# Optimization experiments

Measured on AMD Instinct MI355X. Metric: run time of the kernel, lower is better.

The kernel has to match this reference:

```python
import jax, jax.numpy as jnp
import numpy as np

N_NODE, N_USER, N_PRICE, EMB = 100000, 40000, 100, 128
E_VV, E_VP, E_VU, E_UV = 2000000, 200000, 2000000, 2000000


def _spmm(rows, cols, vals, x, n_rows):
    # sparse COO (n_rows, n_cols) @ x  -> (n_rows, d)
    return jax.ops.segment_sum(vals[:, None] * x[cols], rows, num_segments=n_rows)


def _row_norm_spmm(rows, cols, vals, x, n_rows):
    # torch.sparse.mm followed by division by row-sum of values (+1e-8)
    num = _spmm(rows, cols, vals, x, n_rows)
    den = jax.ops.segment_sum(vals, rows, num_segments=n_rows)[:, None] + 1e-8
    return num / den


def _linear(x, W, b):
    return x @ W.T + b


def setup_inputs() -> dict:
    key = jax.random.key(0)
    ks = jax.random.split(key, 40)
    d = {}
    d['embedding'] = jax.random.normal(ks[0], (N_NODE, EMB), jnp.float32) * 0.1
    d['pri_emb'] = jax.random.normal(ks[1], (N_PRICE, EMB), jnp.float32) * 0.1
    d['user_emb'] = jax.random.normal(ks[2], (N_USER, EMB), jnp.float32) * 0.1
    d['adj_rows'] = jax.random.randint(ks[3], (E_VV,), 0, N_NODE, jnp.int32)
    d['adj_cols'] = jax.random.randint(ks[4], (E_VV,), 0, N_NODE, jnp.int32)
    d['adj_vals'] = jax.random.uniform(ks[5], (E_VV,), jnp.float32)
    d['vp_rows'] = jax.random.randint(ks[6], (E_VP,), 0, N_NODE, jnp.int32)
    d['vp_cols'] = jax.random.randint(ks[7], (E_VP,), 0, N_PRICE, jnp.int32)
    d['vp_vals'] = jax.random.uniform(ks[8], (E_VP,), jnp.float32)
    d['vu_rows'] = jax.random.randint(ks[9], (E_VU,), 0, N_NODE, jnp.int32)
    d['vu_cols'] = jax.random.randint(ks[10], (E_VU,), 0, N_USER, jnp.int32)
    d['vu_vals'] = jax.random.uniform(ks[11], (E_VU,), jnp.float32)
    d['pv_rows'] = jax.random.randint(ks[12], (E_VP,), 0, N_PRICE, jnp.int32)
    d['pv_cols'] = jax.random.randint(ks[13], (E_VP,), 0, N_NODE, jnp.int32)
    d['pv_vals'] = jax.random.uniform(ks[14], (E_VP,), jnp.float32)
    d['uv_rows'] = jax.random.randint(ks[15], (E_UV,), 0, N_USER, jnp.int32)
    d['uv_cols'] = jax.random.randint(ks[16], (E_UV,), 0, N_NODE, jnp.int32)
    d['uv_vals'] = jax.random.uniform(ks[17], (E_UV,), jnp.float32)
    d['item_price_indices'] = jax.random.randint(ks[18], (N_NODE,), 0, N_PRICE, jnp.int32)
    s = 0.02
    d['mat_vu'] = jax.random.normal(ks[19], (N_NODE, 1), jnp.float32) * s
    d['mat_pv'] = jax.random.normal(ks[20], (N_PRICE, 1), jnp.float32) * s
    d['mat_uv'] = jax.random.normal(ks[21], (N_USER, 1), jnp.float32) * s
    d['W_aogi'] = jax.random.normal(ks[22], (EMB, 2 * EMB), jnp.float32) * s
    d['b_aogi'] = jnp.zeros((EMB,), jnp.float32)
    d['W_bgi1'] = jax.random.normal(ks[23], (EMB, EMB), jnp.float32) * s
    d['b_bgi1'] = jnp.zeros((EMB,), jnp.float32)
    d['W_aogp'] = jax.random.normal(ks[24], (EMB, 2 * EMB), jnp.float32) * s
    d['b_aogp'] = jnp.zeros((EMB,), jnp.float32)
    d['W_bgp1'] = jax.random.normal(ks[25], (EMB, EMB), jnp.float32) * s
    d['b_bgp1'] = jnp.zeros((EMB,), jnp.float32)
    d['W_user'] = jax.random.normal(ks[26], (EMB, 3 * EMB), jnp.float32) * s
    d['b_user'] = jnp.zeros((EMB,), jnp.float32)
    d['user_lambda'] = jnp.asarray(0.2, jnp.float32)
    return d


def _forward(embedding, pri_emb, user_emb,
             adj_rows, adj_cols, adj_vals,
             vp_rows, vp_cols, vp_vals,
             vu_rows, vu_cols, vu_vals,
             pv_rows, pv_cols, pv_vals,
             uv_rows, uv_cols, uv_vals,
             item_price_indices,
             mat_vu, mat_pv, mat_uv,
             W_aogi, b_aogi, W_bgi1, b_bgi1,
             W_aogp, b_aogp, W_bgp1, b_bgp1,
             W_user, b_user, user_lambda,
             layers=1):
    def inter_gate(Wa, ba, Wb, bb, e1, e2):
        gate = jax.nn.sigmoid(_linear(jnp.concatenate([e1, e2], 1), Wa, ba) + _linear(e1, Wb, bb))
        return e1 + gate * e2  # dropout50 = identity at eval

    def intra_gate(rows, cols, vals, mat_v, emb2, n_rows):
        # torch version computes the chunked row-normalized spmm under no_grad
        alpha = jax.lax.stop_gradient(_row_norm_spmm(rows, cols, vals, emb2, n_rows))
        return alpha * mat_v  # dropout70 = identity at eval

    for _ in range(layers):
        item = (inter_gate(W_aogi, b_aogi, W_bgi1, b_bgi1, embedding,
                           _spmm(vp_rows, vp_cols, vp_vals, pri_emb, N_NODE))
                + _spmm(adj_rows, adj_cols, adj_vals, embedding, N_NODE)
                + user_lambda * intra_gate(vu_rows, vu_cols, vu_vals, mat_vu, user_emb, N_NODE))
        price = inter_gate(W_aogp, b_aogp, W_bgp1, b_bgp1, pri_emb,
                           intra_gate(pv_rows, pv_cols, pv_vals, mat_pv, embedding, N_PRICE))
        e_price_user = _spmm(uv_rows, uv_cols, uv_vals, pri_emb[item_price_indices], N_USER)
        e_item_user = intra_gate(uv_rows, uv_cols, uv_vals, mat_uv, embedding, N_USER)
        gate = jax.nn.sigmoid(_linear(jnp.concatenate([user_emb, e_item_user, e_price_user], -1), W_user, b_user))
        user = gate * user_emb + (1.0 - gate) * e_item_user
        embedding, pri_emb, user_emb = item, price, user
    return item, price, user


def reference(embedding, pri_emb, user_emb,
              adj_rows, adj_cols, adj_vals,
              vp_rows, vp_cols, vp_vals,
              vu_rows, vu_cols, vu_vals,
              pv_rows, pv_cols, pv_vals,
              uv_rows, uv_cols, uv_vals,
              item_price_indices,
              mat_vu, mat_pv, mat_uv,
              W_aogi, b_aogi, W_bgi1, b_bgi1,
              W_aogp, b_aogp, W_bgp1, b_bgp1,
              W_user, b_user, user_lambda):
    return _forward(embedding, pri_emb, user_emb,
                    adj_rows, adj_cols, adj_vals,
                    vp_rows, vp_cols, vp_vals,
                    vu_rows, vu_cols, vu_vals,
                    pv_rows, pv_cols, pv_vals,
                    uv_rows, uv_cols, uv_vals,
                    item_price_indices,
                    mat_vu, mat_pv, mat_uv,
                    W_aogi, b_aogi, W_bgi1, b_bgi1,
                    W_aogp, b_aogp, W_bgp1, b_bgp1,
                    W_user, b_user, user_lambda)
```

## Files before the change

### kernel.cpp

```cpp
#include <hip/hip_runtime.h>
#include <hip/hip_bf16.h>

#define N_NODE 100000
#define N_USER 40000
#define N_PRICE 100
#define EMB 128
#define E_VV 2000000
#define E_VP 200000
#define E_VU 2000000
#define E_UV 2000000

#define FOFF0 0
#define FOFF1 256
#define FOFF2 512
#define FOFF3 767
#define FOFF4 1023
#define FTOT  1073
#define EPB   8192
#define BK1 245
#define BK2 490
#define BK3 735
#define BK4 760
#define BKT 785
#define CB1 256
#define CB2 512
#define CB3 767
#define CB4 1023
#define CBT 1073
#define RB_PV   100
#define RB_ITEM 25000
#define RB_USER 10000
#define RBT (RB_PV + RB_ITEM + RB_USER)
#define FB_ITEM 782
#define FB_USER 313
#define FBT (FB_ITEM + FB_USER + 50)

typedef __attribute__((ext_vector_type(8))) short short8;
typedef __attribute__((ext_vector_type(4))) float f32x4;

__device__ __forceinline__ float sigf(float x){ return 1.f/(1.f+__expf(-x)); }
__device__ __forceinline__ unsigned bfr(float f){
  unsigned u = __float_as_uint(f);
  return (u + 0x7FFFu + ((u>>16)&1u)) >> 16;
}
__device__ __forceinline__ float bf_lo(unsigned u){ return __uint_as_float(u << 16); }
__device__ __forceinline__ float bf_hi(unsigned u){ return __uint_as_float(u & 0xFFFF0000u); }
__device__ __forceinline__ unsigned pack2(float x, float y){ return bfr(x) | (bfr(y)<<16); }

__global__ __launch_bounds__(256) void k_cvt_all(
    const float4* __restrict__ se, const float4* __restrict__ su, const float4* __restrict__ sp,
    uint2* __restrict__ de, uint2* __restrict__ du, uint2* __restrict__ dp){
  const int nE = N_NODE*EMB/4, nU = N_USER*EMB/4, nP = N_PRICE*EMB/4;
  int i = blockIdx.x*256 + threadIdx.x;
  const float4* src; uint2* dst; int j;
  if (i < nE){ src = se; dst = de; j = i; }
  else if (i < nE+nU){ src = su; dst = du; j = i-nE; }
  else if (i < nE+nU+nP){ src = sp; dst = dp; j = i-nE-nU; }
  else return;
  float4 v = src[j];
  dst[j] = make_uint2(bfr(v.x) | (bfr(v.y)<<16), bfr(v.z) | (bfr(v.w)<<16));
}

__global__ __launch_bounds__(256) void k_prep(
    const float* __restrict__ Wa, const float* __restrict__ Wb, const float* __restrict__ Wu,
    ushort* __restrict__ Wc, ushort* __restrict__ Wub,
    int* __restrict__ fill,
    int2* __restrict__ adjE, int2* __restrict__ vuE, int2* __restrict__ uvE,
    int2* __restrict__ vpE, int2* __restrict__ pvE){
  if (blockIdx.x == 320){
    int t = threadIdx.x;
    for (int i = t; i < FTOT; i += 256) fill[i] = 0;
    if (t < 16){
      int2 z = make_int2(0,0);
      adjE[E_VV+t] = z; vuE[E_VU+t] = z; uvE[E_UV+t] = z; vpE[E_VP+t] = z; pvE[E_VP+t] = z;
    }
    return;
  }
  int idx = blockIdx.x*256 + threadIdx.x;
  if (idx < 128*256){
    int n = idx >> 8, k = idx & 255;
    float v = Wa[n*256+k] + ((k < 128) ? Wb[n*128+k] : 0.f);
    Wc[idx] = (ushort)bfr(v);
  } else {
    int j = idx - 128*256;
    if (j < 128*384) Wub[j] = (ushort)bfr(Wu[j]);
  }
}

template<int E, int RPB, int NB, int CAPc>
__device__ __forceinline__ void bucket_body(int blk,
    const int* __restrict__ rows, const int* __restrict__ cols, const float* __restrict__ vals,
    int* __restrict__ fill, uint2* __restrict__ stg, int* cnt, int* gbase)
{
  const int t = threadIdx.x;
  const int e0 = blk * EPB;
  for (int i = t; i < NB; i += 256) cnt[i] = 0;
  __syncthreads();
  int rr[32];
  #pragma unroll
  for (int i = 0; i < 32; ++i){
    int e = e0 + i*256 + t;
    rr[i] = (e < E) ? rows[e] : -1;
    if (rr[i] >= 0) atomicAdd(&cnt[rr[i]/RPB], 1);
  }
  __syncthreads();
  for (int b = t; b < NB; b += 256){
    int c = cnt[b];
    gbase[b] = (c > 0) ? atomicAdd(&fill[b], c) : 0;
    cnt[b] = 0;
  }
  __syncthreads();
  #pragma unroll
  for (int i = 0; i < 32; ++i){
    if (rr[i] >= 0){
      int e = e0 + i*256 + t;
      int b = rr[i]/RPB, rl = rr[i] - b*RPB;
      int slot = gbase[b] + atomicAdd(&cnt[b], 1);
      if (slot >= CAPc) slot = CAPc - 1;
      stg[(size_t)b*CAPc + slot] = make_uint2((unsigned)cols[e] | ((unsigned)rl << 17), __float_as_uint(vals[e]));
    }
  }
}

__global__ __launch_bounds__(256) void k_bucket_all(
    const int* __restrict__ aR, const int* __restrict__ aC, const float* __restrict__ aV,
    const int* __restrict__ uR, const int* __restrict__ uC, const float* __restrict__ uV,
    const int* __restrict__ vR, const int* __restrict__ vC, const float* __restrict__ vV,
    const int* __restrict__ pR, const int* __restrict__ pC, const float* __restrict__ pV,
    const int* __restrict__ qR, const int* __restrict__ qC, const float* __restrict__ qV,
    int* __restrict__ fill,
    uint2* __restrict__ stgA, uint2* __restrict__ stgU, uint2* __restrict__ stgV,
    uint2* __restrict__ stgP, uint2* __restrict__ stgQ)
{
  __shared__ int cnt[256], gbase[256];
  int b = blockIdx.x;
  if      (b < BK1) bucket_body<E_VV,391,256,8704>(b,      aR,aC,aV, fill+FOFF0, stgA, cnt, gbase);
  else if (b < BK2) bucket_body<E_VU,391,256,8704>(b-BK1,  uR,uC,uV, fill+FOFF1, stgU, cnt, gbase);
  else if (b < BK3) bucket_body<E_UV,157,255,8704>(b-BK2,  vR,vC,vV, fill+FOFF2, stgV, cnt, gbase);
  else if (b < BK4) bucket_body<E_VP,391,256,1536>(b-BK3,  pR,pC,pV, fill+FOFF3, stgP, cnt, gbase);
  else              bucket_body<E_VP,  2, 50,5120>(b-BK4,  qR,qC,qV, fill+FOFF4, stgQ, cnt, gbase);
}

template<int NROW, int RPB, int NB, int CAPc>
__device__ __forceinline__ void csr_body(int b,
    const uint2* __restrict__ stg, const int* __restrict__ fill,
    int* __restrict__ start, int2* __restrict__ csr,
    int* cnt, uint2* stage, int* sbase)
{
  const int t = threadIdx.x;
  const int row0 = b * RPB;
  int R = NROW - row0; if (R > RPB) R = RPB;
  int count = fill[b]; if (count > CAPc) count = CAPc;
  for (int i = t; i < R; i += 256) cnt[i] = 0;
  if (t < 64){
    int run = 0;
    for (int c0 = 0; c0 < NB; c0 += 64){
      int j = c0 + t;
      int x = (j < NB) ? fill[j] : 0;
      int s = x;
      #pragma unroll
      for (int d = 1; d < 64; d <<= 1){ int y = __shfl_up(s, d); if (t >= d) s += y; }
      if (j == b) *sbase = run + s - x;
      run += __shfl(s, 63);
    }
  }
  __syncthreads();
  const int base = *sbase;
  const uint2* mystg = stg + (size_t)b*CAPc;
  for (int j = t; j < count; j += 256)
    atomicAdd(&cnt[mystg[j].x >> 17], 1);
  __syncthreads();
  if (t < 64){
    int run = 0;
    for (int c0 = 0; c0 < R; c0 += 64){
      int i = c0 + t;
      int x = (i < R) ? cnt[i] : 0;
      int s = x;
      #pragma unroll
      for (int d = 1; d < 64; d <<= 1){ int y = __shfl_up(s, d); if (t >= d) s += y; }
      if (i < R) cnt[i] = run + s - x;
      run += __shfl(s, 63);
    }
  }
  __syncthreads();
  for (int i = t; i < R; i += 256) start[row0 + i] = base + cnt[i];
  if (b == NB-1 && t == 0) start[NROW] = base + count;
  __syncthreads();
  for (int j = t; j < count; j += 256){
    uint2 kv = mystg[j];
    int rl = kv.x >> 17;
    int pos = atomicAdd(&cnt[rl], 1);
    stage[pos] = kv;
  }
  __syncthreads();
  for (int j = t; j < count; j += 256){
    uint2 kv = stage[j];
    csr[base + j] = make_int2((int)(kv.x & 0x1FFFF), (int)kv.y);
  }
}

__global__ __launch_bounds__(256) void k_csr_all(
    const uint2* __restrict__ stgA, const uint2* __restrict__ stgU, const uint2* __restrict__ stgV,
    const uint2* __restrict__ stgP, const uint2* __restrict__ stgQ,
    const int* __restrict__ fill,
    int* __restrict__ aS, int* __restrict__ uS, int* __restrict__ vS,
    int* __restrict__ pS, int* __restrict__ qS,
    int2* __restrict__ aE, int2* __restrict__ uE, int2* __restrict__ vE,
    int2* __restrict__ pE, int2* __restrict__ qE)
{
  __shared__ int cnt[391];
  __shared__ int sbase;
  __shared__ uint2 stage[8704];
  int b = blockIdx.x;
  if      (b < CB1) csr_body<N_NODE,391,256,8704>(b,     stgA, fill+FOFF0, aS, aE, cnt, stage, &sbase);
  else if (b < CB2) csr_body<N_NODE,391,256,8704>(b-CB1, stgU, fill+FOFF1, uS, uE, cnt, stage, &sbase);
  else if (b < CB3) csr_body<N_USER,157,255,8704>(b-CB2, stgV, fill+FOFF2, vS, vE, cnt, stage, &sbase);
  else if (b < CB4) csr_body<N_NODE,391,256,1536>(b-CB3, stgP, fill+FOFF3, pS, pE, cnt, stage, &sbase);
  else              csr_body<N_PRICE,  2, 50,5120>(b-CB4, stgQ, fill+FOFF4, qS, qE, cnt, stage, &sbase);
}


#define FMA8(ACC, U, V)                                     \
  ACC[0] += (V)*bf_lo((U).x); ACC[1] += (V)*bf_hi((U).x);   \
  ACC[2] += (V)*bf_lo((U).y); ACC[3] += (V)*bf_hi((U).y);   \
  ACC[4] += (V)*bf_lo((U).z); ACC[5] += (V)*bf_hi((U).z);   \
  ACC[6] += (V)*bf_lo((U).w); ACC[7] += (V)*bf_hi((U).w);

#define RED8(ACC)                                           \
  _Pragma("unroll")                                         \
  for (int j = 0; j < 8; ++j){                              \
    ACC[j] += __shfl_xor(ACC[j], 16);                       \
    ACC[j] += __shfl_xor(ACC[j], 32);                       \
  }

__device__ __forceinline__ void item_body(int rb,
    const uint4* __restrict__ be4, const uint4* __restrict__ bu4, const uint4* __restrict__ bp4,
    const int* __restrict__ aS, const int2* __restrict__ aE,
    const int* __restrict__ uS, const int2* __restrict__ uE,
    const int* __restrict__ pS, const int2* __restrict__ pE,
    const float* __restrict__ mat_vu, const float* __restrict__ lam,
    float4* __restrict__ out4, uint4* __restrict__ vp4)
{
  const int r = rb*4 + (threadIdx.x >> 6);
  const int l = threadIdx.x & 63;
  const int g = l >> 4, q = l & 15;
  float aA[8] = {}, aU[8] = {}, aP[8] = {};
  float den = 0.f;
  int s = aS[r], e = aS[r+1];
  for (int i = s; i < e; i += 16){
    int2 cv[4]; uint4 u[4];
    #pragma unroll
    for (int k = 0; k < 4; ++k) cv[k] = aE[i + 4*k + g];
    #pragma unroll
    for (int k = 0; k < 4; ++k) u[k] = be4[(size_t)cv[k].x*16 + q];
    #pragma unroll
    for (int k = 0; k < 4; ++k){
      float v = (i + 4*k + g < e) ? __int_as_float(cv[k].y) : 0.f;
      FMA8(aA, u[k], v)
    }
  }
  s = uS[r]; e = uS[r+1];
  for (int i = s; i < e; i += 16){
    int2 cv[4]; uint4 u[4];
    #pragma unroll
    for (int k = 0; k < 4; ++k) cv[k] = uE[i + 4*k + g];
    #pragma unroll
    for (int k = 0; k < 4; ++k) u[k] = bu4[(size_t)cv[k].x*16 + q];
    #pragma unroll
    for (int k = 0; k < 4; ++k){
      float v = (i + 4*k + g < e) ? __int_as_float(cv[k].y) : 0.f;
      FMA8(aU, u[k], v)
      den += v;
    }
  }
  s = pS[r]; e = pS[r+1];
  for (int i = s; i < e; i += 16){
    int2 cv[4]; uint4 u[4];
    #pragma unroll
    for (int k = 0; k < 4; ++k) cv[k] = pE[i + 4*k + g];
    #pragma unroll
    for (int k = 0; k < 4; ++k) u[k] = bp4[(size_t)cv[k].x*16 + q];
    #pragma unroll
    for (int k = 0; k < 4; ++k){
      float v = (i + 4*k + g < e) ? __int_as_float(cv[k].y) : 0.f;
      FMA8(aP, u[k], v)
    }
  }
  RED8(aA) RED8(aU) RED8(aP)
  den += __shfl_xor(den, 16); den += __shfl_xor(den, 32);
  float sc = lam[0]*mat_vu[r]/(den + 1e-8f);
  if (g == 0){
    out4[(size_t)r*32 + q*2]     = make_float4(aA[0]+sc*aU[0], aA[1]+sc*aU[1], aA[2]+sc*aU[2], aA[3]+sc*aU[3]);
    out4[(size_t)r*32 + q*2 + 1] = make_float4(aA[4]+sc*aU[4], aA[5]+sc*aU[5], aA[6]+sc*aU[6], aA[7]+sc*aU[7]);
    vp4[(size_t)r*16 + q] = make_uint4(pack2(aP[0],aP[1]), pack2(aP[2],aP[3]), pack2(aP[4],aP[5]), pack2(aP[6],aP[7]));
  }
}

__device__ __forceinline__ void user_body(int rb,
    const uint4* __restrict__ be4, const uint4* __restrict__ bp4,
    const int* __restrict__ S, const int2* __restrict__ E,
    const int* __restrict__ ipi, const float* __restrict__ mat_uv,
    uint4* __restrict__ eit4, uint4* __restrict__ uvp4)
{
  const int r = rb*4 + (threadIdx.x >> 6);
  const int l = threadIdx.x & 63;
  const int g = l >> 4, q = l & 15;
  float aI[8] = {}, aP[8] = {};
  float den = 0.f;
  int s = S[r], e = S[r+1];
  for (int i = s; i < e; i += 8){
    int2 cv[2];
    #pragma unroll
    for (int k = 0; k < 2; ++k) cv[k] = E[i + 4*k + g];
    uint4 u[2]; int ip[2];
    #pragma unroll
    for (int k = 0; k < 2; ++k){ u[k] = be4[(size_t)cv[k].x*16 + q]; ip[k] = ipi[cv[k].x]; }
    uint4 y[2];
    #pragma unroll
    for (int k = 0; k < 2; ++k) y[k] = bp4[(size_t)ip[k]*16 + q];
    #pragma unroll
    for (int k = 0; k < 2; ++k){
      float v = (i + 4*k + g < e) ? __int_as_float(cv[k].y) : 0.f;
      FMA8(aI, u[k], v)
      FMA8(aP, y[k], v)
      den += v;
    }
  }
  RED8(aI) RED8(aP)
  den += __shfl_xor(den, 16); den += __shfl_xor(den, 32);
  float sc = mat_uv[r]/(den + 1e-8f);
  if (g == 0){
    eit4[(size_t)r*16 + q] = make_uint4(pack2(sc*aI[0],sc*aI[1]), pack2(sc*aI[2],sc*aI[3]),
                                        pack2(sc*aI[4],sc*aI[5]), pack2(sc*aI[6],sc*aI[7]));
    uvp4[(size_t)r*16 + q] = make_uint4(pack2(aP[0],aP[1]), pack2(aP[2],aP[3]),
                                        pack2(aP[4],aP[5]), pack2(aP[6],aP[7]));
  }
}

__device__ __forceinline__ void pv_body(int r,
    const uint4* __restrict__ be4, const int2* __restrict__ E, const int* __restrict__ S,
    float* __restrict__ num, float* __restrict__ den_out)
{
  const int t = threadIdx.x;
  const int wid = t >> 6, l = t & 63;
  const int g = l >> 4, q = l & 15;
  float aP[8] = {}; float den = 0.f;
  int s = S[r], e = S[r+1];
  for (int i0 = s + wid*16; i0 < e; i0 += 64){
    int2 cv[4]; uint4 u[4];
    #pragma unroll
    for (int k = 0; k < 4; ++k) cv[k] = E[i0 + 4*k + g];
    #pragma unroll
    for (int k = 0; k < 4; ++k) u[k] = be4[(size_t)cv[k].x*16 + q];
    #pragma unroll
    for (int k = 0; k < 4; ++k){
      float v = (i0 + 4*k + g < e) ? __int_as_float(cv[k].y) : 0.f;
      FMA8(aP, u[k], v)
      den += v;
    }
  }
  RED8(aP)
  den += __shfl_xor(den, 16); den += __shfl_xor(den, 32);
  __shared__ float red[4][16][8];
  __shared__ float dred[4];
  if (g == 0){
    #pragma unroll
    for (int j = 0; j < 8; ++j) red[wid][q][j] = aP[j];
    if (l == 0) dred[wid] = den;
  }
  __syncthreads();
  if (t < 16){
    #pragma unroll
    for (int j = 0; j < 8; ++j)
      num[r*128 + t*8 + j] = red[0][t][j] + red[1][t][j] + red[2][t][j] + red[3][t][j];
    if (t == 0) den_out[r] = dred[0] + dred[1] + dred[2] + dred[3];
  }
}

__global__ __launch_bounds__(256) void k_rows_all(
    const uint4* __restrict__ be4, const uint4* __restrict__ bu4, const uint4* __restrict__ bp4,
    const int* __restrict__ aS, const int2* __restrict__ aE,
    const int* __restrict__ uS, const int2* __restrict__ uE,
    const int* __restrict__ pS, const int2* __restrict__ pE,
    const int* __restrict__ vS, const int2* __restrict__ vE,
    const int* __restrict__ qS, const int2* __restrict__ qE,
    const int* __restrict__ ipi,
    const float* __restrict__ mat_vu, const float* __restrict__ mat_uv, const float* __restrict__ lam,
    float4* __restrict__ out4, uint4* __restrict__ vp4,
    uint4* __restrict__ eit4, uint4* __restrict__ uvp4,
    float* __restrict__ pv_num, float* __restrict__ pv_den)
{
  int b = blockIdx.x;
  if (b < RB_PV){ pv_body(b, be4, qE, qS, pv_num, pv_den); return; }
  b -= RB_PV;
  if (b < RB_ITEM){ item_body(b, be4, bu4, bp4, aS, aE, uS, uE, pS, pE, mat_vu, lam, out4, vp4); return; }
  b -= RB_ITEM;
  user_body(b, be4, bp4, vS, vE, ipi, mat_uv, eit4, uvp4);
}

__device__ __forceinline__ void item_final_body(int blk, ushort* As, ushort* Bs,
    const ushort* __restrict__ A0, const ushort* __restrict__ A1,
    const ushort* __restrict__ W,
    const float* __restrict__ ba, const float* __restrict__ bb,
    const float* __restrict__ emb, float* __restrict__ out)
{
  const int t = threadIdx.x;
  const int l = t & 63, wv = t >> 6;
  const int wr = (wv>>1)*64, wc = (wv&1)*64;
  const int row0 = blk*128;
  const int lr16 = t >> 3;
  const int slot = t & 7;
  f32x4 acc[4][4] = {};
  for (int s = 0; s < 4; ++s){
    if (s) __syncthreads();
    const int k0 = s*64;
    const ushort* srcA = (k0 < 128) ? (A0 + k0) : (A1 + (k0 - 128));
    #pragma unroll
    for (int i = 0; i < 4; ++i){
      int r = i*32 + lr16;
      int gr = row0 + r; if (gr >= N_NODE) gr = N_NODE-1;
      uint4 va = *(const uint4*)(srcA + (size_t)gr*128 + slot*8);
      *(uint4*)&As[r*64 + ((slot*8) ^ ((r&7)*8))] = va;
      uint4 vb = *(const uint4*)(W + r*256 + k0 + slot*8);
      *(uint4*)&Bs[r*64 + ((slot*8) ^ ((r&7)*8))] = vb;
    }
    __syncthreads();
    #pragma unroll
    for (int kk = 0; kk < 64; kk += 32){
      short8 af[4], bf[4];
      #pragma unroll
      for (int f = 0; f < 4; ++f){
        int ar = wr + f*16 + (l&15);
        af[f] = *(const short8*)&As[ar*64 + ((kk + (l>>4)*8) ^ ((ar&7)*8))];
        int bn = wc + f*16 + (l&15);
        bf[f] = *(const short8*)&Bs[bn*64 + ((kk + (l>>4)*8) ^ ((bn&7)*8))];
      }
      #pragma unroll
      for (int fi = 0; fi < 4; ++fi)
        #pragma unroll
        for (int fj = 0; fj < 4; ++fj)
          acc[fi][fj] = __builtin_amdgcn_mfma_f32_16x16x32_bf16(af[fi], bf[fj], acc[fi][fj], 0, 0, 0);
    }
  }
  const int g4 = (l>>4)*4;
  #pragma unroll
  for (int fi = 0; fi < 4; ++fi){
    #pragma unroll
    for (int r = 0; r < 4; ++r){
      int grow = row0 + wr + fi*16 + g4 + r;
      if (grow < N_NODE){
        #pragma unroll
        for (int fj = 0; fj < 4; ++fj){
          int col = wc + fj*16 + (l&15);
          float x = acc[fi][fj][r] + ba[col] + bb[col];
          unsigned pv2 = *(const unsigned*)&A1[(size_t)grow*128 + (col & ~1)];
          float v = (col & 1) ? bf_hi(pv2) : bf_lo(pv2);
          size_t o = (size_t)grow*128 + col;
          out[o] = emb[o] + sigf(x)*v + out[o];
        }
      }
    }
  }
}

__device__ __forceinline__ void user_final_body(int blk, ushort* As, ushort* Bs,
    const ushort* __restrict__ A0, const ushort* __restrict__ A1, const ushort* __restrict__ A2,
    const ushort* __restrict__ W,
    const float* __restrict__ bu,
    const float* __restrict__ ue, float* __restrict__ out)
{
  const int t = threadIdx.x;
  const int l = t & 63, wv = t >> 6;
  const int wr = (wv>>1)*64, wc = (wv&1)*64;
  const int row0 = blk*128;
  const int lr16 = t >> 3;
  const int slot = t & 7;
  f32x4 acc[4][4] = {};
  for (int s = 0; s < 6; ++s){
    if (s) __syncthreads();
    const int k0 = s*64;
    const ushort* base = (s < 2) ? A0 : ((s < 4) ? A1 : A2);
    const ushort* srcA = base + (s & 1)*64;
    #pragma unroll
    for (int i = 0; i < 4; ++i){
      int r = i*32 + lr16;
      int gr = row0 + r; if (gr >= N_USER) gr = N_USER-1;
      uint4 va = *(const uint4*)(srcA + (size_t)gr*128 + slot*8);
      *(uint4*)&As[r*64 + ((slot*8) ^ ((r&7)*8))] = va;
      uint4 vb = *(const uint4*)(W + r*384 + k0 + slot*8);
      *(uint4*)&Bs[r*64 + ((slot*8) ^ ((r&7)*8))] = vb;
    }
    __syncthreads();
    #pragma unroll
    for (int kk = 0; kk < 64; kk += 32){
      short8 af[4], bf[4];
      #pragma unroll
      for (int f = 0; f < 4; ++f){
        int ar = wr + f*16 + (l&15);
        af[f] = *(const short8*)&As[ar*64 + ((kk + (l>>4)*8) ^ ((ar&7)*8))];
        int bn = wc + f*16 + (l&15);
        bf[f] = *(const short8*)&Bs[bn*64 + ((kk + (l>>4)*8) ^ ((bn&7)*8))];
      }
      #pragma unroll
      for (int fi = 0; fi < 4; ++fi)
        #pragma unroll
        for (int fj = 0; fj < 4; ++fj)
          acc[fi][fj] = __builtin_amdgcn_mfma_f32_16x16x32_bf16(af[fi], bf[fj], acc[fi][fj], 0, 0, 0);
    }
  }
  const int g4 = (l>>4)*4;
  #pragma unroll
  for (int fi = 0; fi < 4; ++fi){
    #pragma unroll
    for (int r = 0; r < 4; ++r){
      int grow = row0 + wr + fi*16 + g4 + r;
      if (grow < N_USER){
        #pragma unroll
        for (int fj = 0; fj < 4; ++fj){
          int col = wc + fj*16 + (l&15);
          float g = sigf(acc[fi][fj][r] + bu[col]);
          unsigned e2 = *(const unsigned*)&A1[(size_t)grow*128 + (col & ~1)];
          float ei = (col & 1) ? bf_hi(e2) : bf_lo(e2);
          size_t o = (size_t)grow*128 + col;
          out[o] = g*ue[o] + (1.f - g)*ei;
        }
      }
    }
  }
}

__device__ __forceinline__ void price_final_body(int blk, float* A2,
    const float* __restrict__ pe, const float* __restrict__ num, const float* __restrict__ den,
    const float* __restrict__ mat_pv,
    const float* __restrict__ Wa, const float* __restrict__ ba,
    const float* __restrict__ Wb, const float* __restrict__ bb,
    float* __restrict__ out_price)
{
  int t = threadIdx.x;
  #pragma unroll
  for (int i = 0; i < 2; ++i){
    int flat = i*256 + t;
    int rl = flat >> 8; int k = flat & 255;
    int r = blk*2 + rl;
    float v;
    if (k < 128) v = pe[r*128 + k];
    else         v = num[r*128 + (k-128)] / (den[r] + 1e-8f) * mat_pv[r];
    A2[rl*256 + k] = v;
  }
  __syncthreads();
  int rl = t >> 7; int c = t & 127;
  int r = blk*2 + rl;
  float x = 0.f;
  #pragma unroll 4
  for (int k = 0; k < 256; ++k){
    float w = (k < 128) ? (Wa[c*256 + k] + Wb[c*128 + k]) : Wa[c*256 + k];
    x += A2[rl*256 + k]*w;
  }
  float g = sigf(x + ba[c] + bb[c]);
  out_price[r*128 + c] = pe[r*128 + c] + g*A2[rl*256 + 128 + c];
}

__global__ __launch_bounds__(256) void k_finals_all(
    const ushort* __restrict__ bemb, const ushort* __restrict__ vp_bf, const ushort* __restrict__ Wc,
    const float* __restrict__ b_aogi, const float* __restrict__ b_bgi1,
    const float* __restrict__ emb, float* __restrict__ out_item,
    const ushort* __restrict__ bue, const ushort* __restrict__ eitem_bf, const ushort* __restrict__ uvp_bf,
    const ushort* __restrict__ Wub, const float* __restrict__ b_user,
    const float* __restrict__ ue, float* __restrict__ out_user,
    const float* __restrict__ pe, const float* __restrict__ pv_num, const float* __restrict__ pv_den,
    const float* __restrict__ mat_pv,
    const float* __restrict__ W_aogp, const float* __restrict__ b_aogp,
    const float* __restrict__ W_bgp1, const float* __restrict__ b_bgp1,
    float* __restrict__ out_price)
{
  __shared__ __align__(16) ushort As[128*64];
  __shared__ __align__(16) ushort Bs[128*64];
  __shared__ float A2[512];
  int b = blockIdx.x;
  if (b < FB_ITEM){
    item_final_body(b, As, Bs, bemb, vp_bf, Wc, b_aogi, b_bgi1, emb, out_item);
  } else if (b < FB_ITEM + FB_USER){
    user_final_body(b - FB_ITEM, As, Bs, bue, eitem_bf, uvp_bf, Wub, b_user, ue, out_user);
  } else {
    price_final_body(b - FB_ITEM - FB_USER, A2, pe, pv_num, pv_den, mat_pv,
                     W_aogp, b_aogp, W_bgp1, b_bgp1, out_price);
  }
}

extern "C" void kernel_launch(void* const* d_in, const int* in_sizes, int n_in,
                              void* d_out, int out_size, void* d_ws, size_t ws_size,
                              hipStream_t stream){
  (void)in_sizes; (void)n_in; (void)out_size; (void)ws_size;
  const float* emb = (const float*)d_in[0];
  const float* pe  = (const float*)d_in[1];
  const float* ue  = (const float*)d_in[2];
  const int*   adj_r = (const int*)d_in[3];  const int* adj_c = (const int*)d_in[4];  const float* adj_v = (const float*)d_in[5];
  const int*   vp_r  = (const int*)d_in[6];  const int* vp_c  = (const int*)d_in[7];  const float* vp_v  = (const float*)d_in[8];
  const int*   vu_r  = (const int*)d_in[9];  const int* vu_c  = (const int*)d_in[10]; const float* vu_v  = (const float*)d_in[11];
  const int*   pv_r  = (const int*)d_in[12]; const int* pv_c  = (const int*)d_in[13]; const float* pv_v  = (const float*)d_in[14];
  const int*   uv_r  = (const int*)d_in[15]; const int* uv_c  = (const int*)d_in[16]; const float* uv_v  = (const float*)d_in[17];
  const int*   ipi   = (const int*)d_in[18];
  const float* mat_vu = (const float*)d_in[19];
  const float* mat_pv = (const float*)d_in[20];
  const float* mat_uv = (const float*)d_in[21];
  const float* W_aogi = (const float*)d_in[22]; const float* b_aogi = (const float*)d_in[23];
  const float* W_bgi1 = (const float*)d_in[24]; const float* b_bgi1 = (const float*)d_in[25];
  const float* W_aogp = (const float*)d_in[26]; const float* b_aogp = (const float*)d_in[27];
  const float* W_bgp1 = (const float*)d_in[28]; const float* b_bgp1 = (const float*)d_in[29];
  const float* W_user = (const float*)d_in[30]; const float* b_user = (const float*)d_in[31];
  const float* lam    = (const float*)d_in[32];

  float* out_item  = (float*)d_out;
  float* out_price = out_item + (size_t)N_NODE*EMB;
  float* out_user  = out_price + (size_t)N_PRICE*EMB;

  char* w = (char*)d_ws;
  size_t off = 0;
  auto alloc = [&](size_t bytes)->char*{
    char* p = w + off;
    off = (off + bytes + 255) & ~(size_t)255;
    return p;
  };
  int* fill = (int*)alloc(FTOT*4);
  int* aS  = (int*)alloc((N_NODE+1)*4);
  int* uS  = (int*)alloc((N_NODE+1)*4);
  int* vS  = (int*)alloc((N_USER+1)*4);
  int* pS  = (int*)alloc((N_NODE+1)*4);
  int* qS  = (int*)alloc(101*4);
  ushort* Wc_item = (ushort*)alloc(128*256*2);
  ushort* Wu_bf   = (ushort*)alloc(128*384*2);
  char* region = alloc((size_t)93*1024*1024);
  uint2* stgA = (uint2*)region;
  uint2* stgU = (uint2*)(region + (size_t)256*8704*8);
  uint2* stgV = (uint2*)(region + (size_t)2*256*8704*8);
  uint2* stgP = (uint2*)(region + (size_t)3*256*8704*8);
  uint2* stgQ = (uint2*)(region + (size_t)3*256*8704*8 + (size_t)256*1536*8);
  unsigned* bemb = (unsigned*)region;
  unsigned* bue  = (unsigned*)(region + (size_t)N_NODE*EMB*2);
  unsigned* bpe  = (unsigned*)(region + (size_t)(N_NODE+N_USER)*EMB*2);
  unsigned* vp_bf = (unsigned*)(region + (size_t)37*1024*1024);
  int2*  adjE = (int2*)alloc(((size_t)E_VV+16)*8);
  int2*  vuE  = (int2*)alloc(((size_t)E_VU+16)*8);
  int2*  uvE  = (int2*)alloc(((size_t)E_UV+16)*8);
  int2*  vpE  = (int2*)alloc(((size_t)E_VP+16)*8);
  int2*  pvE  = (int2*)alloc(((size_t)E_VP+16)*8);
  unsigned* eitem_bf = (unsigned*)alloc((size_t)N_USER*64*4);
  unsigned* uvp_bf   = (unsigned*)alloc((size_t)N_USER*64*4);
  float* pv_num   = (float*)alloc((size_t)N_PRICE*EMB*4);
  float* pv_den   = (float*)alloc(N_PRICE*4);

  k_prep<<<321,256,0,stream>>>(W_aogi, W_bgi1, W_user, Wc_item, Wu_bf,
                               fill, adjE, vuE, uvE, vpE, pvE);

  k_bucket_all<<<BKT,256,0,stream>>>(
      adj_r,adj_c,adj_v, vu_r,vu_c,vu_v, uv_r,uv_c,uv_v, vp_r,vp_c,vp_v, pv_r,pv_c,pv_v,
      fill, stgA, stgU, stgV, stgP, stgQ);

  k_csr_all<<<CBT,256,0,stream>>>(stgA, stgU, stgV, stgP, stgQ, fill,
      aS, uS, vS, pS, qS, adjE, vuE, uvE, vpE, pvE);

  k_cvt_all<<<((N_NODE+N_USER+N_PRICE)*EMB/4+255)/256,256,0,stream>>>(
      (const float4*)emb, (const float4*)ue, (const float4*)pe,
      (uint2*)bemb, (uint2*)bue, (uint2*)bpe);

  k_rows_all<<<RBT,256,0,stream>>>(
      (const uint4*)bemb, (const uint4*)bue, (const uint4*)bpe,
      aS, adjE, uS, vuE, pS, vpE, vS, uvE, qS, pvE,
      ipi, mat_vu, mat_uv, lam,
      (float4*)out_item, (uint4*)vp_bf, (uint4*)eitem_bf, (uint4*)uvp_bf,
      pv_num, pv_den);

  k_finals_all<<<FBT,256,0,stream>>>(
      (const ushort*)bemb, (const ushort*)vp_bf, Wc_item, b_aogi, b_bgi1, emb, out_item,
      (const ushort*)bue, (const ushort*)eitem_bf, (const ushort*)uvp_bf, Wu_bf, b_user, ue, out_user,
      pe, pv_num, pv_den, mat_pv, W_aogp, b_aogp, W_bgp1, b_bgp1, out_price);
}
```

Before: 588.0 us.

## Pad bucket chunks to 16 entries and sort CSR rows by column sub-bins

Bucket staging now reserves 16-aligned chunks per block, filling the gaps with marker entries, and tracks padded and real counts separately. The CSR build sorts each row's edges into 16 column sub-bins, so later gathers within a row touch nearby columns. The aim is better locality in the SpMM gather and aligned staging writes. The cost is a larger staging capacity, more shared memory (a 6256-entry bin array, which lowers occupancy), extra marker writes, and a second atomic per bucket.

```diff
diff --git a/kernel.cpp b/kernel.cpp
--- a/kernel.cpp
+++ b/kernel.cpp
@@ -35,6 +35,9 @@
 #define FB_USER 313
 #define FBT (FB_ITEM + FB_USER + 50)
 
+#define CAPA 12032
+#define MARK 0xFFFFFFFFu
+
 typedef __attribute__((ext_vector_type(8))) short short8;
 typedef __attribute__((ext_vector_type(4))) float f32x4;
 
@@ -69,7 +72,7 @@
     int2* __restrict__ vpE, int2* __restrict__ pvE){
   if (blockIdx.x == 320){
     int t = threadIdx.x;
-    for (int i = t; i < FTOT; i += 256) fill[i] = 0;
+    for (int i = t; i < 2*FTOT; i += 256) fill[i] = 0;
     if (t < 16){
       int2 z = make_int2(0,0);
       adjE[E_VV+t] = z; vuE[E_VU+t] = z; uvE[E_UV+t] = z; vpE[E_VP+t] = z; pvE[E_VP+t] = z;
@@ -90,7 +93,8 @@
 template<int E, int RPB, int NB, int CAPc>
 __device__ __forceinline__ void bucket_body(int blk,
     const int* __restrict__ rows, const int* __restrict__ cols, const float* __restrict__ vals,
-    int* __restrict__ fill, uint2* __restrict__ stg, int* cnt, int* gbase)
+    int* __restrict__ fillPad, int* __restrict__ fillReal,
+    uint2* __restrict__ stg, int* cnt, int* gbase)
 {
   const int t = threadIdx.x;
   const int e0 = blk * EPB;
@@ -106,7 +110,17 @@
   __syncthreads();
   for (int b = t; b < NB; b += 256){
     int c = cnt[b];
-    gbase[b] = (c > 0) ? atomicAdd(&fill[b], c) : 0;
+    int gb = 0;
+    if (c > 0){
+      int rounded = (c + 15) & ~15;
+      gb = atomicAdd(&fillPad[b], rounded);
+      atomicAdd(&fillReal[b], c);
+      for (int j = c; j < rounded; ++j){
+        int slot = gb + j; if (slot >= CAPc) slot = CAPc - 1;
+        stg[(size_t)b*CAPc + slot] = make_uint2(MARK, 0u);
+      }
+    }
+    gbase[b] = gb;
     cnt[b] = 0;
   }
   __syncthreads();
@@ -128,35 +142,35 @@
     const int* __restrict__ vR, const int* __restrict__ vC, const float* __restrict__ vV,
     const int* __restrict__ pR, const int* __restrict__ pC, const float* __restrict__ pV,
     const int* __restrict__ qR, const int* __restrict__ qC, const float* __restrict__ qV,
-    int* __restrict__ fill,
+    int* __restrict__ fillPad, int* __restrict__ fillReal,
     uint2* __restrict__ stgA, uint2* __restrict__ stgU, uint2* __restrict__ stgV,
     uint2* __restrict__ stgP, uint2* __restrict__ stgQ)
 {
   __shared__ int cnt[256], gbase[256];
   int b = blockIdx.x;
-  if      (b < BK1) bucket_body<E_VV,391,256,8704>(b,      aR,aC,aV, fill+FOFF0, stgA, cnt, gbase);
-  else if (b < BK2) bucket_body<E_VU,391,256,8704>(b-BK1,  uR,uC,uV, fill+FOFF1, stgU, cnt, gbase);
-  else if (b < BK3) bucket_body<E_UV,157,255,8704>(b-BK2,  vR,vC,vV, fill+FOFF2, stgV, cnt, gbase);
-  else if (b < BK4) bucket_body<E_VP,391,256,1536>(b-BK3,  pR,pC,pV, fill+FOFF3, stgP, cnt, gbase);
-  else              bucket_body<E_VP,  2, 50,5120>(b-BK4,  qR,qC,qV, fill+FOFF4, stgQ, cnt, gbase);
-}
-
-template<int NROW, int RPB, int NB, int CAPc>
+  if      (b < BK1) bucket_body<E_VV,391,256,CAPA>(b,      aR,aC,aV, fillPad+FOFF0, fillReal+FOFF0, stgA, cnt, gbase);
+  else if (b < BK2) bucket_body<E_VU,391,256,CAPA>(b-BK1,  uR,uC,uV, fillPad+FOFF1, fillReal+FOFF1, stgU, cnt, gbase);
+  else if (b < BK3) bucket_body<E_UV,157,255,CAPA>(b-BK2,  vR,vC,vV, fillPad+FOFF2, fillReal+FOFF2, stgV, cnt, gbase);
+  else if (b < BK4) bucket_body<E_VP,391,256,1536>(b-BK3,  pR,pC,pV, fillPad+FOFF3, fillReal+FOFF3, stgP, cnt, gbase);
+  else              bucket_body<E_VP,  2, 50,5632>(b-BK4,  qR,qC,qV, fillPad+FOFF4, fillReal+FOFF4, stgQ, cnt, gbase);
+}
+
+template<int NROW, int RPB, int NB, int CAPc, int BINS>
 __device__ __forceinline__ void csr_body(int b,
-    const uint2* __restrict__ stg, const int* __restrict__ fill,
+    const uint2* __restrict__ stg, const int* __restrict__ fillPad, const int* __restrict__ fillReal,
     int* __restrict__ start, int2* __restrict__ csr,
-    int* cnt, uint2* stage, int* sbase)
+    int* cnt2, uint2* stage, int* sbase, int* stot)
 {
   const int t = threadIdx.x;
   const int row0 = b * RPB;
   int R = NROW - row0; if (R > RPB) R = RPB;
-  int count = fill[b]; if (count > CAPc) count = CAPc;
-  for (int i = t; i < R; i += 256) cnt[i] = 0;
+  int cpad = fillPad[b]; if (cpad > CAPc) cpad = CAPc;
+  for (int i = t; i < BINS; i += 256) cnt2[i] = 0;
   if (t < 64){
     int run = 0;
     for (int c0 = 0; c0 < NB; c0 += 64){
       int j = c0 + t;
-      int x = (j < NB) ? fill[j] : 0;
+      int x = (j < NB) ? fillReal[j] : 0;
       int s = x;
       #pragma unroll
       for (int d = 1; d < 64; d <<= 1){ int y = __shfl_up(s, d); if (t >= d) s += y; }
@@ -167,33 +181,40 @@
   __syncthreads();
   const int base = *sbase;
   const uint2* mystg = stg + (size_t)b*CAPc;
-  for (int j = t; j < count; j += 256)
-    atomicAdd(&cnt[mystg[j].x >> 17], 1);
+  for (int j = t; j < cpad; j += 256){
+    unsigned x = mystg[j].x;
+    if (x != MARK)
+      atomicAdd(&cnt2[((x >> 17) << 4) | ((x & 0x1FFFFu) >> 13)], 1);
+  }
   __syncthreads();
   if (t < 64){
     int run = 0;
-    for (int c0 = 0; c0 < R; c0 += 64){
+    for (int c0 = 0; c0 < BINS; c0 += 64){
       int i = c0 + t;
-      int x = (i < R) ? cnt[i] : 0;
+      int x = (i < BINS) ? cnt2[i] : 0;
       int s = x;
       #pragma unroll
       for (int d = 1; d < 64; d <<= 1){ int y = __shfl_up(s, d); if (t >= d) s += y; }
-      if (i < R) cnt[i] = run + s - x;
+      if (i < BINS) cnt2[i] = run + s - x;
       run += __shfl(s, 63);
     }
-  }
-  __syncthreads();
-  for (int i = t; i < R; i += 256) start[row0 + i] = base + cnt[i];
-  if (b == NB-1 && t == 0) start[NROW] = base + count;
-  __syncthreads();
-  for (int j = t; j < count; j += 256){
+    if (t == 0) *stot = run;
+  }
+  __syncthreads();
+  const int creal = *stot;
+  for (int i = t; i < R; i += 256) start[row0 + i] = base + cnt2[i*16];
+  if (b == NB-1 && t == 0) start[NROW] = base + creal;
+  __syncthreads();
+  for (int j = t; j < cpad; j += 256){
     uint2 kv = mystg[j];
-    int rl = kv.x >> 17;
-    int pos = atomicAdd(&cnt[rl], 1);
-    stage[pos] = kv;
-  }
-  __syncthreads();
-  for (int j = t; j < count; j += 256){
+    if (kv.x != MARK){
+      int key = ((kv.x >> 17) << 4) | ((kv.x & 0x1FFFFu) >> 13);
+      int pos = atomicAdd(&cnt2[key], 1);
+      stage[pos] = kv;
+    }
+  }
+  __syncthreads();
+  for (int j = t; j < creal; j += 256){
     uint2 kv = stage[j];
     csr[base + j] = make_int2((int)(kv.x & 0x1FFFF), (int)kv.y);
   }
@@ -202,21 +223,21 @@
 __global__ __launch_bounds__(256) void k_csr_all(
     const uint2* __restrict__ stgA, const uint2* __restrict__ stgU, const uint2* __restrict__ stgV,
     const uint2* __restrict__ stgP, const uint2* __restrict__ stgQ,
-    const int* __restrict__ fill,
+    const int* __restrict__ fillPad, const int* __restrict__ fillReal,
     int* __restrict__ aS, int* __restrict__ uS, int* __restrict__ vS,
     int* __restrict__ pS, int* __restrict__ qS,
     int2* __restrict__ aE, int2* __restrict__ uE, int2* __restrict__ vE,
     int2* __restrict__ pE, int2* __restrict__ qE)
 {
-  __shared__ int cnt[391];
-  __shared__ int sbase;
+  __shared__ int cnt2[6256];
+  __shared__ int sbase, stot;
   __shared__ uint2 stage[8704];
   int b = blockIdx.x;
-  if      (b < CB1) csr_body<N_NODE,391,256,8704>(b,     stgA, fill+FOFF0, aS, aE, cnt, stage, &sbase);
-  else if (b < CB2) csr_body<N_NODE,391,256,8704>(b-CB1, stgU, fill+FOFF1, uS, uE, cnt, stage, &sbase);
-  else if (b < CB3) csr_body<N_USER,157,255,8704>(b-CB2, stgV, fill+FOFF2, vS, vE, cnt, stage, &sbase);
-  else if (b < CB4) csr_body<N_NODE,391,256,1536>(b-CB3, stgP, fill+FOFF3, pS, pE, cnt, stage, &sbase);
-  else              csr_body<N_PRICE,  2, 50,5120>(b-CB4, stgQ, fill+FOFF4, qS, qE, cnt, stage, &sbase);
+  if      (b < CB1) csr_body<N_NODE,391,256,CAPA,6256>(b,     stgA, fillPad+FOFF0, fillReal+FOFF0, aS, aE, cnt2, stage, &sbase, &stot);
+  else if (b < CB2) csr_body<N_NODE,391,256,CAPA,6256>(b-CB1, stgU, fillPad+FOFF1, fillReal+FOFF1, uS, uE, cnt2, stage, &sbase, &stot);
+  else if (b < CB3) csr_body<N_USER,157,255,CAPA,2512>(b-CB2, stgV, fillPad+FOFF2, fillReal+FOFF2, vS, vE, cnt2, stage, &sbase, &stot);
+  else if (b < CB4) csr_body<N_NODE,391,256,1536,6256>(b-CB3, stgP, fillPad+FOFF3, fillReal+FOFF3, pS, pE, cnt2, stage, &sbase, &stot);
+  else              csr_body<N_PRICE,  2, 50,5632,  32>(b-CB4, stgQ, fillPad+FOFF4, fillReal+FOFF4, qS, qE, cnt2, stage, &sbase, &stot);
 }
 
 
@@ -621,7 +642,8 @@
     off = (off + bytes + 255) & ~(size_t)255;
     return p;
   };
-  int* fill = (int*)alloc(FTOT*4);
+  int* fillPad  = (int*)alloc(2*FTOT*4);
+  int* fillReal = fillPad + FTOT;
   int* aS  = (int*)alloc((N_NODE+1)*4);
   int* uS  = (int*)alloc((N_NODE+1)*4);
   int* vS  = (int*)alloc((N_USER+1)*4);
@@ -631,10 +653,10 @@
   ushort* Wu_bf   = (ushort*)alloc(128*384*2);
   char* region = alloc((size_t)93*1024*1024);
   uint2* stgA = (uint2*)region;
-  uint2* stgU = (uint2*)(region + (size_t)256*8704*8);
-  uint2* stgV = (uint2*)(region + (size_t)2*256*8704*8);
-  uint2* stgP = (uint2*)(region + (size_t)3*256*8704*8);
-  uint2* stgQ = (uint2*)(region + (size_t)3*256*8704*8 + (size_t)256*1536*8);
+  uint2* stgU = (uint2*)(region + (size_t)256*CAPA*8);
+  uint2* stgV = (uint2*)(region + (size_t)2*256*CAPA*8);
+  uint2* stgP = (uint2*)(region + (size_t)3*256*CAPA*8);
+  uint2* stgQ = (uint2*)(region + (size_t)3*256*CAPA*8 + (size_t)256*1536*8);
   unsigned* bemb = (unsigned*)region;
   unsigned* bue  = (unsigned*)(region + (size_t)N_NODE*EMB*2);
   unsigned* bpe  = (unsigned*)(region + (size_t)(N_NODE+N_USER)*EMB*2);
@@ -650,13 +672,13 @@
   float* pv_den   = (float*)alloc(N_PRICE*4);
 
   k_prep<<<321,256,0,stream>>>(W_aogi, W_bgi1, W_user, Wc_item, Wu_bf,
-                               fill, adjE, vuE, uvE, vpE, pvE);
+                               fillPad, adjE, vuE, uvE, vpE, pvE);
 
   k_bucket_all<<<BKT,256,0,stream>>>(
       adj_r,adj_c,adj_v, vu_r,vu_c,vu_v, uv_r,uv_c,uv_v, vp_r,vp_c,vp_v, pv_r,pv_c,pv_v,
-      fill, stgA, stgU, stgV, stgP, stgQ);
-
-  k_csr_all<<<CBT,256,0,stream>>>(stgA, stgU, stgV, stgP, stgQ, fill,
+      fillPad, fillReal, stgA, stgU, stgV, stgP, stgQ);
+
+  k_csr_all<<<CBT,256,0,stream>>>(stgA, stgU, stgV, stgP, stgQ, fillPad, fillReal,
       aS, uS, vS, pS, qS, adjE, vuE, uvE, vpE, pvE);
 
   k_cvt_all<<<((N_NODE+N_USER+N_PRICE)*EMB/4+255)/256,256,0,stream>>>(
```

Result: slower. 720.6 us (+22.6%).
